# Performance work log

Hardware: AMD Instinct MI355X
Metric: run time of the kernel (lower is better)

The kernel has to match this reference:

```python
import jax, jax.numpy as jnp
import numpy as np

B, T, C, N = 4, 1024, 1024, 64
H = C // N
# dims = [max(32, 32*round(fac*C**p/32))] per module formula for C=1024
D_W, D_A, D_V, D_G = 64, 64, 32, 160
GN_EPS = 0.00064


def setup_inputs() -> dict:
    key = jax.random.key(0)
    keys = iter(jax.random.split(key, 40))

    def rn(shape, s=0.02):
        return jax.random.normal(next(keys), shape, jnp.float32) * s

    return {
        "x": jax.random.normal(next(keys), (B, T, C), jnp.float32),
        "v_first": jax.random.normal(next(keys), (B, T, C), jnp.float32),
        "x_r": rn((1, 1, C), 0.5), "x_w": rn((1, 1, C), 0.5), "x_k": rn((1, 1, C), 0.5),
        "x_v": rn((1, 1, C), 0.5), "x_a": rn((1, 1, C), 0.5), "x_g": rn((1, 1, C), 0.5),
        "w0": rn((1, 1, C), 0.5) - 1.0, "w1": rn((C, D_W)), "w2": rn((D_W, C)),
        "a0": rn((1, 1, C), 0.5), "a1": rn((C, D_A)), "a2": rn((D_A, C)),
        "v0p": rn((1, 1, C), 0.5), "v1": rn((C, D_V)), "v2": rn((D_V, C)),
        "g1": rn((C, D_G)), "g2": rn((D_G, C)),
        "k_k": rn((1, 1, C), 0.2) + 0.8, "k_a": rn((1, 1, C), 0.2) + 1.0,
        "r_k": rn((H, N), 0.5),
        "W_r": rn((C, C)), "W_k": rn((C, C)), "W_v": rn((C, C)), "W_o": rn((C, C)),
        "gn_w": jnp.ones((C,), jnp.float32), "gn_b": jnp.zeros((C,), jnp.float32),
    }


def _group_norm(x2, wgt, bias):
    # torch GroupNorm(H groups, C channels) on [B*T, C]: normalize each N-chunk
    xg = x2.reshape(x2.shape[0], H, N)
    mu = xg.mean(-1, keepdims=True)
    var = ((xg - mu) ** 2).mean(-1, keepdims=True)  # biased var, as torch
    xn = (xg - mu) * jax.lax.rsqrt(var + GN_EPS)
    return xn.reshape(x2.shape) * wgt + bias


def rwkv7_recurrence(r, w, k, v, a, b):
    # RWKV-7 chunked-cuda semantics (wind_rwkv naive reference), all [B,T,H,N];
    # w is the per-channel decay exp(-exp(w_raw)) in (0,1).
    # state s: [B,H,N,N], s[i,j] ~ value_i x key_j
    # s_t = s_{t-1} * diag(w_t) + (s_{t-1} @ a_t) outer b_t + v_t outer k_t
    # y_t = s_t @ r_t
    def step(s, inp):
        r_t, w_t, k_t, v_t, a_t, b_t = inp  # each [B,H,N]
        sa = jnp.einsum('bhij,bhj->bhi', s, a_t)
        s = (s * w_t[:, :, None, :]
             + sa[..., None] * b_t[:, :, None, :]
             + v_t[..., None] * k_t[:, :, None, :])
        y = jnp.einsum('bhij,bhj->bhi', s, r_t)
        return s, y

    xs = tuple(jnp.swapaxes(t, 0, 1) for t in (r, w, k, v, a, b))  # [T,B,H,N]
    s0 = jnp.zeros((r.shape[0], r.shape[2], r.shape[3], r.shape[3]), r.dtype)
    _, ys = jax.lax.scan(step, s0, xs)
    return jnp.swapaxes(ys, 0, 1)  # [B,T,H,N]


def reference(x, v_first, x_r, x_w, x_k, x_v, x_a, x_g, w0, w1, w2, a0, a1, a2,
              v0p, v1, v2, g1, g2, k_k, k_a, r_k, W_r, W_k, W_v, W_o, gn_w, gn_b):
    Bx, Tx, Cx = x.shape
    # F.pad(x, (0,0,1,-1)): shift tokens right by one, zero at t=0
    last_x = jnp.concatenate([jnp.zeros_like(x[:, :1]), x[:, :-1]], axis=1)
    dx = last_x - x
    xr, xw, xk, xv, xa, xg = (x + m * dx for m in (x_r, x_w, x_k, x_v, x_a, x_g))
    r = xr @ W_r.T
    w = -jax.nn.softplus(-w0 - jnp.tanh(xw @ w1) @ w2) - 0.5
    k = xk @ W_k.T
    v = xv @ W_v.T
    v = v + (v_first - v) * jax.nn.sigmoid(v0p + (xv @ v1) @ v2)
    a = jax.nn.sigmoid(a0 + (xa @ a1) @ a2)
    g = jax.nn.sigmoid(xg @ g1) @ g2
    kk = k * k_k
    k = k * (1.0 + (a - 1.0) * k_a)
    rs, ws, ks, vs, kks, aa = (t.reshape(Bx, Tx, H, N) for t in (r, w, k, v, kk, a))
    # F.normalize(kk, dim=-1) with eps clamp 1e-12
    kks = kks / jnp.maximum(jnp.linalg.norm(kks, axis=-1, keepdims=True), 1e-12)
    wdec = jnp.exp(-jnp.exp(ws))
    y = rwkv7_recurrence(rs, wdec, ks, vs, kks, -kks * aa)  # [B,T,H,N]
    yn = _group_norm(y.reshape(Bx * Tx, Cx), gn_w, gn_b).reshape(Bx, Tx, Cx)
    yn = yn + ((rs * ks * r_k).sum(-1, keepdims=True) * vs).reshape(Bx, Tx, Cx)
    return (yn * g) @ W_o.T
```

## Files before the change

kernel.cpp:

```cpp
#include <hip/hip_runtime.h>
#include <hip/hip_bf16.h>
#include <math.h>


using bf16 = __hip_bfloat16;
typedef __attribute__((ext_vector_type(8))) short bf16x8;
typedef __attribute__((ext_vector_type(4))) float f32x4;

#define DEVINL __device__ __forceinline__

DEVINL float b2f(bf16 v) { return __bfloat162float(v); }
DEVINL bf16 f2b(float f) { return __float2bfloat16(f); }
DEVINL float sigm(float x) { return 1.f / (1.f + __expf(-x)); }
DEVINL float bfbits2f(unsigned short s) { return __uint_as_float(((unsigned)s) << 16); }
DEVINL float lo16(unsigned u) { return __uint_as_float(u << 16); }
DEVINL float hi16(unsigned u) { return __uint_as_float(u & 0xffff0000u); }
DEVINL float ldin(const void* p, size_t i, int fl) {
  return fl ? ((const float*)p)[i] : b2f(((const bf16*)p)[i]);
}

DEVINL void g2lds16(const void* g, void* l) {
  __builtin_amdgcn_global_load_lds(
      (__attribute__((address_space(1))) void*)(g),
      (__attribute__((address_space(3))) void*)(l), 16, 0, 0);
}

DEVINL void wait_vmcnt8() {
  __asm__ volatile("" ::: "memory");
  __builtin_amdgcn_s_waitcnt(0x0F78);
  __asm__ volatile("" ::: "memory");
}

template<int CTRL>
DEVINL float dpp_add(float x) {
  int t = __builtin_amdgcn_update_dpp(0, __float_as_int(x), CTRL, 0xf, 0xf, true);
  return x + __int_as_float(t);
}
DEVINL float rowsum16(float x) {
  x = dpp_add<0x121>(x);
  x = dpp_add<0x122>(x);
  x = dpp_add<0x124>(x);
  x = dpp_add<0x128>(x);
  return x;
}

DEVINL size_t stream_sb(int row, int h) {
  return ((size_t)((row >> 10) * 16 + h) * 1024 + (row & 1023)) * 512;
}
DEVINL size_t slotoff(int n, int s) {
  int u = n * 4 + s;
  return (size_t)(((u >> 3) & 1) * 128 + ((u >> 4) << 3) + (u & 7));
}

__global__ void detect_kernel(const unsigned* __restrict__ x, int* __restrict__ flag) {
  __shared__ int cnt[4];
  int tid = threadIdx.x;
  unsigned w = x[tid];
  float v = fabsf(bfbits2f((unsigned short)(w & 0xffffu)));
  bool plaus = (v >= 1e-4f && v <= 16.f);
  unsigned long long m = __ballot(plaus);
  if ((tid & 63) == 0) cnt[tid >> 6] = __popcll(m);
  __syncthreads();
  if (tid == 0) *flag = (cnt[0] + cnt[1] + cnt[2] + cnt[3] < 128) ? 1 : 0;
}

__global__ __launch_bounds__(256)
void prep_kernel(const void* __restrict__ x,
    const void* mr, const void* mw, const void* mk,
    const void* mv, const void* ma, const void* mg,
    const void* W_r, const void* W_k, const void* W_v, const void* W_o,
    bf16* cWr, bf16* cWk, bf16* cWv, bf16* cWo,
    const void* w1, const void* w2, const void* a1, const void* a2,
    const void* v1, const void* v2, const void* g1, const void* g2,
    bf16* w1t, bf16* w2t, bf16* a1t, bf16* a2t,
    bf16* v1t, bf16* v2t, bf16* g1t, bf16* g2t,
    const int* __restrict__ flag,
    bf16* oxr, bf16* oxw, bf16* oxk, bf16* oxv, bf16* oxa, bf16* oxg)
{
  int fl = *flag;
  int bx = blockIdx.x;
  if (bx < 16384) {
    size_t idx = (size_t)bx * 256 + threadIdx.x;
    int c = (int)(idx & 1023);
    int t = (int)((idx >> 10) & 1023);
    float xc = ldin(x, idx, fl);
    float px = (t == 0) ? 0.f : ldin(x, idx - 1024, fl);
    float dx = px - xc;
    oxr[idx] = f2b(xc + ldin(mr, c, fl) * dx);
    oxw[idx] = f2b(xc + ldin(mw, c, fl) * dx);
    oxk[idx] = f2b(xc + ldin(mk, c, fl) * dx);
    oxv[idx] = f2b(xc + ldin(mv, c, fl) * dx);
    oxa[idx] = f2b(xc + ldin(ma, c, fl) * dx);
    oxg[idx] = f2b(xc + ldin(mg, c, fl) * dx);
  } else if (bx < 32768) {
    int g = (bx - 16384) * 256 + threadIdx.x;
    int seg = g >> 20, i = g & 1048575;
    const void* s = seg == 0 ? W_r : seg == 1 ? W_k : seg == 2 ? W_v : W_o;
    bf16* d = seg == 0 ? cWr : seg == 1 ? cWk : seg == 2 ? cWv : cWo;
    d[i] = fl ? f2b(((const float*)s)[i]) : ((const bf16*)s)[i];
  } else {
    int idx = (bx - 32768) * 256 + threadIdx.x;
    if (idx >= 655360) return;
    const int ends[8] = {65536, 131072, 196608, 262144, 294912, 327680, 491520, 655360};
    const int Ks[8] = {1024, 64, 1024, 64, 1024, 32, 1024, 160};
    const int Nd[8] = {64, 1024, 64, 1024, 32, 1024, 160, 1024};
    const void* srcs[8] = {w1, w2, a1, a2, v1, v2, g1, g2};
    bf16* dsts[8] = {w1t, w2t, a1t, a2t, v1t, v2t, g1t, g2t};
    int seg = 0, start = 0;
#pragma unroll
    for (int s2 = 0; s2 < 7; s2++)
      if (idx >= ends[s2]) { seg = s2 + 1; start = ends[s2]; }
    int local = idx - start;
    int K = Ks[seg], N = Nd[seg];
    int k = local / N, n = local - k * N;
    dsts[seg][(size_t)n * K + k] = f2b(ldin(srcs[seg], local, fl));
  }
}

template<typename Epi>
DEVINL void gemm_core(const bf16* __restrict__ A, const bf16* __restrict__ Bt,
                      int K, int Brows, int m0, int n0, Epi&& epi)
{
  __shared__ short As[128 * 32];
  __shared__ short Bs[128 * 32];
  const int tid = threadIdx.x;
  const int wid = tid >> 6, lane = tid & 63;
  const int wr = (wid >> 1) * 64, wc = (wid & 1) * 64;

  f32x4 acc[4][4] = {};

  const int lrow = lane >> 2;
  const int lcol = (lane & 3) * 8;
  int arow0 = m0 + (wid * 2 + 0) * 16 + lrow;
  int arow1 = m0 + (wid * 2 + 1) * 16 + lrow;
  int brow0 = n0 + (wid * 2 + 0) * 16 + lrow; if (brow0 >= Brows) brow0 = Brows - 1;
  int brow1 = n0 + (wid * 2 + 1) * 16 + lrow; if (brow1 >= Brows) brow1 = Brows - 1;

  const short* Ag = (const short*)A;
  const short* Bg = (const short*)Bt;

  for (int kk = 0; kk < K; kk += 32) {
    __syncthreads();
    g2lds16(Ag + (size_t)arow0 * K + kk + lcol, As + (wid * 2 + 0) * 512);
    g2lds16(Ag + (size_t)arow1 * K + kk + lcol, As + (wid * 2 + 1) * 512);
    g2lds16(Bg + (size_t)brow0 * K + kk + lcol, Bs + (wid * 2 + 0) * 512);
    g2lds16(Bg + (size_t)brow1 * K + kk + lcol, Bs + (wid * 2 + 1) * 512);
    __syncthreads();
    bf16x8 af[4], bfr[4];
#pragma unroll
    for (int mi = 0; mi < 4; mi++)
      af[mi] = *(const bf16x8*)(As + (wr + mi * 16 + (lane & 15)) * 32 + (lane >> 4) * 8);
#pragma unroll
    for (int ni = 0; ni < 4; ni++)
      bfr[ni] = *(const bf16x8*)(Bs + (wc + ni * 16 + (lane & 15)) * 32 + (lane >> 4) * 8);
#pragma unroll
    for (int mi = 0; mi < 4; mi++)
#pragma unroll
      for (int ni = 0; ni < 4; ni++)
        acc[mi][ni] = __builtin_amdgcn_mfma_f32_16x16x32_bf16(af[mi], bfr[ni], acc[mi][ni], 0, 0, 0);
  }

  const int cl0 = lane & 15, r0 = (lane >> 4) * 4;
#pragma unroll
  for (int mi = 0; mi < 4; mi++)
#pragma unroll
    for (int ni = 0; ni < 4; ni++) {
      int col = n0 + wc + ni * 16 + cl0;
#pragma unroll
      for (int rr = 0; rr < 4; rr++)
        epi(m0 + wr + mi * 16 + r0 + rr, col, acc[mi][ni][rr]);
    }
}

__global__ __launch_bounds__(256)
void stage1_kernel(const bf16* xw, const bf16* xa, const bf16* xv, const bf16* xg,
                   const bf16* w1t, const bf16* a1t, const bf16* v1t, const bf16* g1t,
                   bf16* hw, bf16* ha, bf16* hv, bf16* hg)
{
  int y = blockIdx.y;
  int seg = (y <= 2) ? y : 3;
  int n0 = (y == 4) ? 128 : 0;
  const bf16* A  = seg == 0 ? xw  : seg == 1 ? xa  : seg == 2 ? xv  : xg;
  const bf16* Bt = seg == 0 ? w1t : seg == 1 ? a1t : seg == 2 ? v1t : g1t;
  int NS         = seg == 0 ? 64  : seg == 1 ? 64  : seg == 2 ? 32  : 160;
  bf16* out      = seg == 0 ? hw  : seg == 1 ? ha  : seg == 2 ? hv  : hg;
  gemm_core(A, Bt, 1024, NS, blockIdx.x * 128, n0, [&](int row, int col, float f) {
    if (col >= NS) return;
    if (seg == 0) f = tanhf(f);
    else if (seg == 3) f = sigm(f);
    out[(size_t)row * NS + col] = f2b(f);
  });
}

__global__ __launch_bounds__(256)
void bigrkv_kernel(const bf16* xr, const bf16* xk, const bf16* xv,
                   const bf16* cWr, const bf16* cWk, const bf16* cWv,
                   bf16* __restrict__ STR)
{
  int z = blockIdx.z;
  const bf16* A  = z == 0 ? xr  : z == 1 ? xk  : xv;
  const bf16* Bt = z == 0 ? cWr : z == 1 ? cWk : cWv;
  gemm_core(A, Bt, 1024, 1024, blockIdx.x * 128, blockIdx.y * 128,
            [&](int row, int col, float f) {
    size_t sb = stream_sb(row, col >> 6);
    int n = col & 63;
    size_t off = (z == 2) ? (sb + 256 + n) : (sb + slotoff(n, z));
    STR[off] = f2b(f);
  });
}

__global__ __launch_bounds__(256)
void stage2_kernel(const bf16* hw, const bf16* ha, const bf16* hv, const bf16* hg,
                   const bf16* w2t, const bf16* a2t, const bf16* v2t, const bf16* g2t,
                   bf16* __restrict__ STR, float* __restrict__ STRf, float* __restrict__ G,
                   const void* w0, const void* a0, const void* v0p, const void* vfirst,
                   const int* __restrict__ flag)
{
  int fl = *flag;
  int z = blockIdx.z;
  const bf16* A  = z == 0 ? hw  : z == 1 ? ha  : z == 2 ? hv  : hg;
  const bf16* Bt = z == 0 ? w2t : z == 1 ? a2t : z == 2 ? v2t : g2t;
  int K          = z == 0 ? 64  : z == 1 ? 64  : z == 2 ? 32  : 160;
  gemm_core(A, Bt, K, 1024, blockIdx.x * 128, blockIdx.y * 128,
            [&](int row, int col, float f) {
    int n = col & 63;
    if (z == 0) {
      float zz = -(ldin(w0, col, fl) + f);
      float sp = fmaxf(zz, 0.f) + __logf(1.f + __expf(-fabsf(zz)));
      STRf[stream_sb(row, col >> 6) / 2 + 160 + n] = __expf(-__expf(-sp - 0.5f));
    } else if (z == 1) {
      STR[stream_sb(row, col >> 6) + slotoff(n, 2)] = f2b(sigm(ldin(a0, col, fl) + f));
    } else if (z == 2) {
      float sg = sigm(ldin(v0p, col, fl) + f);
      size_t pa = stream_sb(row, col >> 6) + 256 + n;
      float vr = b2f(STR[pa]);
      float vf = ldin(vfirst, (size_t)row * 1024 + col, fl);
      STR[pa] = f2b(vr + (vf - vr) * sg);
    } else {
      G[(size_t)row * 1024 + col] = f;
    }
  });
}

__global__ __launch_bounds__(256)
void post_kernel(bf16* __restrict__ STR, const void* __restrict__ kkw,
                 const void* __restrict__ kaw, const int* __restrict__ flag) {
  int fl = *flag;
  int slot = blockIdx.x * 4 + (threadIdx.x >> 6);
  int tg = slot >> 4, h = slot & 15;
  int n = threadIdx.x & 63, c = h * 64 + n;
  size_t sb = stream_sb(tg, h);
  float kraw = b2f(STR[sb + slotoff(n, 1)]);
  float asig = b2f(STR[sb + slotoff(n, 2)]);
  float kk = kraw * ldin(kkw, c, fl);
  float ss = kk * kk;
  ss += __shfl_xor(ss, 1);  ss += __shfl_xor(ss, 2);  ss += __shfl_xor(ss, 4);
  ss += __shfl_xor(ss, 8);  ss += __shfl_xor(ss, 16); ss += __shfl_xor(ss, 32);
  float kkn = kk / fmaxf(sqrtf(ss), 1e-12f);
  STR[sb + slotoff(n, 2)] = f2b(kkn);
  STR[sb + slotoff(n, 3)] = f2b(-kkn * asig);
  STR[sb + slotoff(n, 1)] = f2b(kraw * (1.f + (asig - 1.f) * ldin(kaw, c, fl)));
}

#define CH 8
__global__ __launch_bounds__(64, 1)
void recur_kernel(const char* __restrict__ STR, float* __restrict__ Y) {
  __shared__ __align__(16) char lds[2 * CH * 1024];
  int blk = blockIdx.x;
  int bh = blk & 63, sib = blk >> 6;
  int b = bh >> 4, h = bh & 15;
  int lane = threadIdx.x;
  int jq = lane & 15, rl = lane >> 4;
  int i = sib * 4 + rl;

  const char* gb = STR + (size_t)bh * (1024 * 1024) + lane * 16;
  float* yout = Y + (size_t)b * 1024 * 1024 + h * 64 + i;

  unsigned lbase = (unsigned)(size_t)(__attribute__((address_space(3))) void*)(void*)lds;
  unsigned lA = lbase + (unsigned)(jq * 16);
  unsigned lB = lbase + 256u + (unsigned)(jq * 16);
  unsigned lV = lbase + 512u + (unsigned)(i * 2);
  unsigned lW = lbase + 640u + (unsigned)(jq * 16);

#pragma unroll
  for (int d = 0; d < CH; ++d)
    g2lds16(gb + (size_t)d * 1024, lds + d * 1024);

  float S0 = 0.f, S1 = 0.f, S2 = 0.f, S3 = 0.f;
  uint4 m0r[2], m1r[2]; float4 wvr[2]; unsigned vur[2];

#define RLOAD(BK, SO) do { \
    unsigned _so = (unsigned)(SO); \
    asm volatile("ds_read_b128 %0, %1" : "=v"(m0r[BK]) : "v"(lA + _so)); \
    asm volatile("ds_read_b128 %0, %1" : "=v"(m1r[BK]) : "v"(lB + _so)); \
    asm volatile("ds_read_b128 %0, %1" : "=v"(wvr[BK]) : "v"(lW + _so)); \
    asm volatile("ds_read_u16  %0, %1" : "=v"(vur[BK]) : "v"(lV + _so)); \
  } while (0)

#define WAITL(N) do { \
    asm volatile("s_waitcnt lgkmcnt(" #N ")" ::: "memory"); \
    __builtin_amdgcn_sched_barrier(0); \
  } while (0)

#define RSTEP(BK, TT) do { \
    uint4 M0 = m0r[BK], M1 = m1r[BK]; float4 WV = wvr[BK]; \
    float vi = lo16(vur[BK]); \
    float rx = lo16(M0.x), kx = hi16(M0.x), ax = lo16(M0.y), bxx = hi16(M0.y); \
    float ry = lo16(M0.z), ky = hi16(M0.z), ay = lo16(M0.w), byy = hi16(M0.w); \
    float rz = lo16(M1.x), kz = hi16(M1.x), az = lo16(M1.y), bzz = hi16(M1.y); \
    float rw2 = lo16(M1.z), kw2 = hi16(M1.z), aw2 = lo16(M1.w), bww = hi16(M1.w); \
    float sa = (S0 * ax + S1 * ay) + (S2 * az + S3 * aw2); \
    sa = rowsum16(sa); \
    S0 = S0 * WV.x + (sa * bxx + vi * kx); \
    S1 = S1 * WV.y + (sa * byy + vi * ky); \
    S2 = S2 * WV.z + (sa * bzz + vi * kz); \
    S3 = S3 * WV.w + (sa * bww + vi * kw2); \
    float yy = (S0 * rx + S1 * ry) + (S2 * rz + S3 * rw2); \
    yy = rowsum16(yy); \
    if (jq == 0) yout[(size_t)(TT) * 1024] = yy; \
  } while (0)

  for (int t0 = 0; t0 < 1024; t0 += CH) {
    int cur = (t0 >> 3) & 1;
    unsigned cbase = (unsigned)(cur * (CH * 1024));
    char* bufn = lds + (cur ^ 1) * (CH * 1024);
#pragma unroll
    for (int d = 0; d < CH; ++d)
      g2lds16(gb + (size_t)(t0 + CH + d) * 1024, bufn + d * 1024);
    wait_vmcnt8();
    RLOAD(0, cbase);
#pragma unroll
    for (int d = 0; d < CH; ++d) {
      if (d + 1 < CH) { RLOAD((d + 1) & 1, cbase + (d + 1) * 1024); WAITL(4); }
      else            { WAITL(0); }
      RSTEP(d & 1, t0 + d);
    }
  }
#undef RLOAD
#undef WAITL
#undef RSTEP
}

__global__ __launch_bounds__(256)
void gn_kernel(const float* __restrict__ Y, const bf16* __restrict__ STR,
               const float* __restrict__ G,
               const void* __restrict__ gw, const void* __restrict__ gb,
               const void* __restrict__ rk, const int* __restrict__ flag,
               bf16* __restrict__ Z)
{
  int fl = *flag;
  int slot = blockIdx.x * 4 + (threadIdx.x >> 6);
  int tg = slot >> 4, h = slot & 15;
  int n = threadIdx.x & 63, c = h * 64 + n;
  size_t sb = stream_sb(tg, h);
  float y = Y[(size_t)tg * 1024 + c];
  float rr = b2f(STR[sb + slotoff(n, 0)]);
  float kf = b2f(STR[sb + slotoff(n, 1)]);
  float vv = b2f(STR[sb + 256 + n]);
  float s1 = y, s2 = y * y, s3 = rr * kf * ldin(rk, c, fl);
#pragma unroll
  for (int m = 1; m < 64; m <<= 1) {
    s1 += __shfl_xor(s1, m);
    s2 += __shfl_xor(s2, m);
    s3 += __shfl_xor(s3, m);
  }
  float mu = s1 * 0.015625f;
  float var = s2 * 0.015625f - mu * mu;
  float xn = (y - mu) * rsqrtf(var + 0.00064f);
  float yn = xn * ldin(gw, c, fl) + ldin(gb, c, fl);
  yn += s3 * vv;
  Z[(size_t)tg * 1024 + c] = f2b(yn * G[(size_t)tg * 1024 + c]);
}

__global__ __launch_bounds__(256)
void outgemm_kernel(const bf16* Z, const bf16* cWo,
                    float* oF, bf16* oB, const int* __restrict__ flag)
{
  int fl = *flag;
  gemm_core(Z, cWo, 1024, 1024, blockIdx.x * 128, blockIdx.y * 128,
            [&](int row, int col, float f) {
    if (fl) oF[(size_t)row * 1024 + col] = f;
    else    oB[(size_t)row * 1024 + col] = f2b(f);
  });
}

extern "C" void kernel_launch(void* const* d_in, const int* in_sizes, int n_in,
                              void* d_out, int out_size, void* d_ws, size_t ws_size,
                              hipStream_t stream)
{
  const void* x      = d_in[0];
  const void* vfirst = d_in[1];
  const void* m_r = d_in[2];  const void* m_w = d_in[3];
  const void* m_k = d_in[4];  const void* m_v = d_in[5];
  const void* m_a = d_in[6];  const void* m_g = d_in[7];
  const void* w0  = d_in[8];  const void* w1  = d_in[9];  const void* w2  = d_in[10];
  const void* a0  = d_in[11]; const void* a1  = d_in[12]; const void* a2  = d_in[13];
  const void* v0p = d_in[14]; const void* v1  = d_in[15]; const void* v2  = d_in[16];
  const void* g1  = d_in[17]; const void* g2  = d_in[18];
  const void* k_k = d_in[19]; const void* k_a = d_in[20]; const void* r_k = d_in[21];
  const void* W_r = d_in[22]; const void* W_k = d_in[23];
  const void* W_v = d_in[24]; const void* W_o = d_in[25];
  const void* gnw = d_in[26]; const void* gnb = d_in[27];
  (void)in_sizes; (void)n_in; (void)out_size; (void)ws_size;

  char* ws = (char*)d_ws;
  size_t off = 0;
  auto alloc = [&](size_t bytes) -> void* {
    void* p = ws + off; off += (bytes + 255) & ~(size_t)255; return p;
  };
  const size_t BTC2 = (size_t)4096 * 1024 * 2;
  int*  flag = (int*)alloc(256);
  bf16* cWr = (bf16*)alloc((size_t)1048576 * 2);
  bf16* cWk = (bf16*)alloc((size_t)1048576 * 2);
  bf16* cWv = (bf16*)alloc((size_t)1048576 * 2);
  bf16* cWo = (bf16*)alloc((size_t)1048576 * 2);
  bf16* w1t = (bf16*)alloc((size_t)65536 * 2);
  bf16* w2t = (bf16*)alloc((size_t)65536 * 2);
  bf16* a1t = (bf16*)alloc((size_t)65536 * 2);
  bf16* a2t = (bf16*)alloc((size_t)65536 * 2);
  bf16* v1t = (bf16*)alloc((size_t)32768 * 2);
  bf16* v2t = (bf16*)alloc((size_t)32768 * 2);
  bf16* g1t = (bf16*)alloc((size_t)163840 * 2);
  bf16* g2t = (bf16*)alloc((size_t)163840 * 2);
  bf16* xr = (bf16*)alloc(BTC2);
  bf16* xw = (bf16*)alloc(BTC2);
  bf16* xk = (bf16*)alloc(BTC2);
  bf16* xv = (bf16*)alloc(BTC2);
  bf16* xa = (bf16*)alloc(BTC2);
  bf16* xg = (bf16*)alloc(BTC2);
  char* STR = (char*)alloc((size_t)64 * 1024 * 1024 + 16384);
  bf16* hw  = (bf16*)alloc((size_t)4096 * 64 * 2);
  bf16* ha  = (bf16*)alloc((size_t)4096 * 64 * 2);
  bf16* hv  = (bf16*)alloc((size_t)4096 * 32 * 2);
  bf16* hg  = (bf16*)alloc((size_t)4096 * 160 * 2);
  float* G = (float*)xr;
  float* Y = (float*)xk;
  bf16*  Z = xa;

  detect_kernel<<<1, 256, 0, stream>>>((const unsigned*)x, flag);
  prep_kernel<<<35328, 256, 0, stream>>>(
      x, m_r, m_w, m_k, m_v, m_a, m_g,
      W_r, W_k, W_v, W_o, cWr, cWk, cWv, cWo,
      w1, w2, a1, a2, v1, v2, g1, g2,
      w1t, w2t, a1t, a2t, v1t, v2t, g1t, g2t,
      flag, xr, xw, xk, xv, xa, xg);

  stage1_kernel<<<dim3(32, 5), 256, 0, stream>>>(xw, xa, xv, xg,
                                                 w1t, a1t, v1t, g1t, hw, ha, hv, hg);
  bigrkv_kernel<<<dim3(32, 8, 3), 256, 0, stream>>>(xr, xk, xv, cWr, cWk, cWv, (bf16*)STR);
  stage2_kernel<<<dim3(32, 8, 4), 256, 0, stream>>>(hw, ha, hv, hg,
                                                    w2t, a2t, v2t, g2t,
                                                    (bf16*)STR, (float*)STR, G,
                                                    w0, a0, v0p, vfirst, flag);
  post_kernel<<<16384, 256, 0, stream>>>((bf16*)STR, k_k, k_a, flag);
  recur_kernel<<<1024, 64, 0, stream>>>(STR, Y);
  gn_kernel<<<16384, 256, 0, stream>>>(Y, (bf16*)STR, G, gnw, gnb, r_k, flag, Z);
  outgemm_kernel<<<dim3(32, 8), 256, 0, stream>>>(Z, cWo, (float*)d_out, (bf16*)d_out, flag);
}
```

Measured before the change: 569.7 us.

## Split recurrence state rows across two half-waves with permlane32 fold

Each recurrence wavefront now holds two state rows, each spread across 32 lanes with two elements per lane, instead of four rows across 16 lanes with four elements each. This doubles the grid to 2048 blocks and adds a permlane32 swap to finish each row reduction. The aim is to shorten the serial per-timestep dependency chain and raise occupancy on the latency-bound scan. The cost is twice as many blocks streaming the same per-head input data from memory, plus an extra cross-lane step per reduction.

```diff
diff --git a/kernel.cpp b/kernel.cpp
--- a/kernel.cpp
+++ b/kernel.cpp
@@ -42,6 +42,11 @@
   x = dpp_add<0x124>(x);
   x = dpp_add<0x128>(x);
   return x;
+}
+DEVINL float fold32(float x) {
+  auto r = __builtin_amdgcn_permlane32_swap(__float_as_int(x), __float_as_int(x),
+                                            false, false);
+  return __int_as_float(r[0]) + __int_as_float(r[1]);
 }
 
 DEVINL size_t stream_sb(int row, int h) {
@@ -263,37 +268,37 @@
 }
 
 #define CH 8
-__global__ __launch_bounds__(64, 1)
+__global__ __launch_bounds__(64, 2)
 void recur_kernel(const char* __restrict__ STR, float* __restrict__ Y) {
   __shared__ __align__(16) char lds[2 * CH * 1024];
   int blk = blockIdx.x;
   int bh = blk & 63, sib = blk >> 6;
   int b = bh >> 4, h = bh & 15;
   int lane = threadIdx.x;
-  int jq = lane & 15, rl = lane >> 4;
-  int i = sib * 4 + rl;
+  int jn = (lane & 15) | ((lane >> 5) << 4);
+  int rl = (lane >> 4) & 1;
+  int i = sib * 2 + rl;
+  int q = jn >> 1, half = jn & 1;
 
   const char* gb = STR + (size_t)bh * (1024 * 1024) + lane * 16;
   float* yout = Y + (size_t)b * 1024 * 1024 + h * 64 + i;
 
   unsigned lbase = (unsigned)(size_t)(__attribute__((address_space(3))) void*)(void*)lds;
-  unsigned lA = lbase + (unsigned)(jq * 16);
-  unsigned lB = lbase + 256u + (unsigned)(jq * 16);
-  unsigned lV = lbase + 512u + (unsigned)(i * 2);
-  unsigned lW = lbase + 640u + (unsigned)(jq * 16);
+  unsigned lRK = lbase + (unsigned)(half * 256 + q * 16);
+  unsigned lV  = lbase + 512u + (unsigned)(i * 2);
+  unsigned lW  = lbase + 640u + (unsigned)(jn * 8);
 
 #pragma unroll
   for (int d = 0; d < CH; ++d)
     g2lds16(gb + (size_t)d * 1024, lds + d * 1024);
 
-  float S0 = 0.f, S1 = 0.f, S2 = 0.f, S3 = 0.f;
-  uint4 m0r[2], m1r[2]; float4 wvr[2]; unsigned vur[2];
+  float S0 = 0.f, S1 = 0.f;
+  uint4 m0r[2]; float2 wvr[2]; unsigned vur[2];
 
 #define RLOAD(BK, SO) do { \
     unsigned _so = (unsigned)(SO); \
-    asm volatile("ds_read_b128 %0, %1" : "=v"(m0r[BK]) : "v"(lA + _so)); \
-    asm volatile("ds_read_b128 %0, %1" : "=v"(m1r[BK]) : "v"(lB + _so)); \
-    asm volatile("ds_read_b128 %0, %1" : "=v"(wvr[BK]) : "v"(lW + _so)); \
+    asm volatile("ds_read_b128 %0, %1" : "=v"(m0r[BK]) : "v"(lRK + _so)); \
+    asm volatile("ds_read_b64  %0, %1" : "=v"(wvr[BK]) : "v"(lW + _so)); \
     asm volatile("ds_read_u16  %0, %1" : "=v"(vur[BK]) : "v"(lV + _so)); \
   } while (0)
 
@@ -303,21 +308,17 @@
   } while (0)
 
 #define RSTEP(BK, TT) do { \
-    uint4 M0 = m0r[BK], M1 = m1r[BK]; float4 WV = wvr[BK]; \
+    uint4 M0 = m0r[BK]; float2 WV = wvr[BK]; \
     float vi = lo16(vur[BK]); \
     float rx = lo16(M0.x), kx = hi16(M0.x), ax = lo16(M0.y), bxx = hi16(M0.y); \
     float ry = lo16(M0.z), ky = hi16(M0.z), ay = lo16(M0.w), byy = hi16(M0.w); \
-    float rz = lo16(M1.x), kz = hi16(M1.x), az = lo16(M1.y), bzz = hi16(M1.y); \
-    float rw2 = lo16(M1.z), kw2 = hi16(M1.z), aw2 = lo16(M1.w), bww = hi16(M1.w); \
-    float sa = (S0 * ax + S1 * ay) + (S2 * az + S3 * aw2); \
-    sa = rowsum16(sa); \
+    float sa = S0 * ax + S1 * ay; \
+    sa = rowsum16(sa); sa = fold32(sa); \
     S0 = S0 * WV.x + (sa * bxx + vi * kx); \
     S1 = S1 * WV.y + (sa * byy + vi * ky); \
-    S2 = S2 * WV.z + (sa * bzz + vi * kz); \
-    S3 = S3 * WV.w + (sa * bww + vi * kw2); \
-    float yy = (S0 * rx + S1 * ry) + (S2 * rz + S3 * rw2); \
-    yy = rowsum16(yy); \
-    if (jq == 0) yout[(size_t)(TT) * 1024] = yy; \
+    float yy = S0 * rx + S1 * ry; \
+    yy = rowsum16(yy); yy = fold32(yy); \
+    if (jn == 0) yout[(size_t)(TT) * 1024] = yy; \
   } while (0)
 
   for (int t0 = 0; t0 < 1024; t0 += CH) {
@@ -331,7 +332,7 @@
     RLOAD(0, cbase);
 #pragma unroll
     for (int d = 0; d < CH; ++d) {
-      if (d + 1 < CH) { RLOAD((d + 1) & 1, cbase + (d + 1) * 1024); WAITL(4); }
+      if (d + 1 < CH) { RLOAD((d + 1) & 1, cbase + (d + 1) * 1024); WAITL(3); }
       else            { WAITL(0); }
       RSTEP(d & 1, t0 + d);
     }
@@ -453,7 +454,7 @@
                                                     (bf16*)STR, (float*)STR, G,
                                                     w0, a0, v0p, vfirst, flag);
   post_kernel<<<16384, 256, 0, stream>>>((bf16*)STR, k_k, k_a, flag);
-  recur_kernel<<<1024, 64, 0, stream>>>(STR, Y);
+  recur_kernel<<<2048, 64, 0, stream>>>(STR, Y);
   gn_kernel<<<16384, 256, 0, stream>>>(Y, (bf16*)STR, G, gnw, gnb, r_k, flag, Z);
   outgemm_kernel<<<dim3(32, 8), 256, 0, stream>>>(Z, cWo, (float*)d_out, (bf16*)d_out, flag);
 }
```

New measurement: 674.6 us. +18.4%, slower.

## Defer y cross-lane reductions and stores out of serial recurrence chain

Applied to the files above, without the earlier changes.

The per-step output y reduction (rowsum16) and global store are moved out of the sequential state-update loop. Partial dot products are kept in registers for a whole chunk, reduced together after the chunk, and stored during the next chunk's iteration. The LDS wait is also rewritten to tie its register operands to the wait instead of using a full sched_barrier, which lets the compiler schedule more freely. This shortens the critical dependency chain per timestep at the cost of extra registers.

```diff
diff --git a/kernel.cpp b/kernel.cpp
--- a/kernel.cpp
+++ b/kernel.cpp
@@ -288,6 +288,8 @@
 
   float S0 = 0.f, S1 = 0.f, S2 = 0.f, S3 = 0.f;
   uint4 m0r[2], m1r[2]; float4 wvr[2]; unsigned vur[2];
+  float yp[CH];
+  float ypR[CH];
 
 #define RLOAD(BK, SO) do { \
     unsigned _so = (unsigned)(SO); \
@@ -297,12 +299,14 @@
     asm volatile("ds_read_u16  %0, %1" : "=v"(vur[BK]) : "v"(lV + _so)); \
   } while (0)
 
-#define WAITL(N) do { \
-    asm volatile("s_waitcnt lgkmcnt(" #N ")" ::: "memory"); \
-    __builtin_amdgcn_sched_barrier(0); \
-  } while (0)
-
-#define RSTEP(BK, TT) do { \
+#define WAITTOK(N, BK) \
+    asm volatile("s_waitcnt lgkmcnt(" #N ")" \
+        : "+v"(m0r[BK].x), "+v"(m0r[BK].y), "+v"(m0r[BK].z), "+v"(m0r[BK].w), \
+          "+v"(m1r[BK].x), "+v"(m1r[BK].y), "+v"(m1r[BK].z), "+v"(m1r[BK].w), \
+          "+v"(wvr[BK].x), "+v"(wvr[BK].y), "+v"(wvr[BK].z), "+v"(wvr[BK].w), \
+          "+v"(vur[BK]))
+
+#define RSTEP(BK, DD) do { \
     uint4 M0 = m0r[BK], M1 = m1r[BK]; float4 WV = wvr[BK]; \
     float vi = lo16(vur[BK]); \
     float rx = lo16(M0.x), kx = hi16(M0.x), ax = lo16(M0.y), bxx = hi16(M0.y); \
@@ -315,9 +319,7 @@
     S1 = S1 * WV.y + (sa * byy + vi * ky); \
     S2 = S2 * WV.z + (sa * bzz + vi * kz); \
     S3 = S3 * WV.w + (sa * bww + vi * kw2); \
-    float yy = (S0 * rx + S1 * ry) + (S2 * rz + S3 * rw2); \
-    yy = rowsum16(yy); \
-    if (jq == 0) yout[(size_t)(TT) * 1024] = yy; \
+    yp[DD] = (S0 * rx + S1 * ry) + (S2 * rz + S3 * rw2); \
   } while (0)
 
   for (int t0 = 0; t0 < 1024; t0 += CH) {
@@ -328,16 +330,28 @@
     for (int d = 0; d < CH; ++d)
       g2lds16(gb + (size_t)(t0 + CH + d) * 1024, bufn + d * 1024);
     wait_vmcnt8();
+    if (t0 && jq == 0) {
+#pragma unroll
+      for (int d = 0; d < CH; ++d)
+        yout[(size_t)(t0 - CH + d) * 1024] = ypR[d];
+    }
     RLOAD(0, cbase);
 #pragma unroll
     for (int d = 0; d < CH; ++d) {
-      if (d + 1 < CH) { RLOAD((d + 1) & 1, cbase + (d + 1) * 1024); WAITL(4); }
-      else            { WAITL(0); }
-      RSTEP(d & 1, t0 + d);
+      if (d + 1 < CH) { RLOAD((d + 1) & 1, cbase + (d + 1) * 1024); WAITTOK(4, d & 1); }
+      else            { WAITTOK(0, d & 1); }
+      RSTEP(d & 1, d);
     }
+#pragma unroll
+    for (int d = 0; d < CH; ++d) ypR[d] = rowsum16(yp[d]);
+  }
+  if (jq == 0) {
+#pragma unroll
+    for (int d = 0; d < CH; ++d)
+      yout[(size_t)(1024 - CH + d) * 1024] = ypR[d];
   }
 #undef RLOAD
-#undef WAITL
+#undef WAITTOK
 #undef RSTEP
 }
 
```

Result: slower. 600.8 us (+5.4%).

## Transpose recurrence output, relax vmcnt wait, and use register-token LDS waits

Applied to the files above, without the earlier changes.

The recurrence kernel now writes y in a transposed [b, channel, t] layout, so each channel's outputs across time are contiguous, and the group-norm kernel reads from that layout. The global-to-LDS prefetch wait is relaxed after the first chunk (vmcnt 16), letting more prefetches stay in flight. The LDS wait no longer uses a full sched_barrier; instead it ties only the needed registers to the waitcnt so the compiler can schedule more freely. The risk is strided gathers in the gn kernel, and possible reordering hazards if the register tokens miss a dependency.

```diff
diff --git a/kernel.cpp b/kernel.cpp
--- a/kernel.cpp
+++ b/kernel.cpp
@@ -28,6 +28,11 @@
 DEVINL void wait_vmcnt8() {
   __asm__ volatile("" ::: "memory");
   __builtin_amdgcn_s_waitcnt(0x0F78);
+  __asm__ volatile("" ::: "memory");
+}
+DEVINL void wait_vmcnt16() {
+  __asm__ volatile("" ::: "memory");
+  __builtin_amdgcn_s_waitcnt(0x4F70);
   __asm__ volatile("" ::: "memory");
 }
 
@@ -264,7 +269,7 @@
 
 #define CH 8
 __global__ __launch_bounds__(64, 1)
-void recur_kernel(const char* __restrict__ STR, float* __restrict__ Y) {
+void recur_kernel(const char* __restrict__ STR, float* __restrict__ Yt) {
   __shared__ __align__(16) char lds[2 * CH * 1024];
   int blk = blockIdx.x;
   int bh = blk & 63, sib = blk >> 6;
@@ -274,7 +279,7 @@
   int i = sib * 4 + rl;
 
   const char* gb = STR + (size_t)bh * (1024 * 1024) + lane * 16;
-  float* yout = Y + (size_t)b * 1024 * 1024 + h * 64 + i;
+  float* yout = Yt + ((size_t)b * 1024 + h * 64 + i) * 1024;
 
   unsigned lbase = (unsigned)(size_t)(__attribute__((address_space(3))) void*)(void*)lds;
   unsigned lA = lbase + (unsigned)(jq * 16);
@@ -297,10 +302,12 @@
     asm volatile("ds_read_u16  %0, %1" : "=v"(vur[BK]) : "v"(lV + _so)); \
   } while (0)
 
-#define WAITL(N) do { \
-    asm volatile("s_waitcnt lgkmcnt(" #N ")" ::: "memory"); \
-    __builtin_amdgcn_sched_barrier(0); \
-  } while (0)
+#define WAITTOK(N, BK) \
+    asm volatile("s_waitcnt lgkmcnt(" #N ")" \
+        : "+v"(m0r[BK].x), "+v"(m0r[BK].y), "+v"(m0r[BK].z), "+v"(m0r[BK].w), \
+          "+v"(m1r[BK].x), "+v"(m1r[BK].y), "+v"(m1r[BK].z), "+v"(m1r[BK].w), \
+          "+v"(wvr[BK].x), "+v"(wvr[BK].y), "+v"(wvr[BK].z), "+v"(wvr[BK].w), \
+          "+v"(vur[BK]))
 
 #define RSTEP(BK, TT) do { \
     uint4 M0 = m0r[BK], M1 = m1r[BK]; float4 WV = wvr[BK]; \
@@ -317,7 +324,7 @@
     S3 = S3 * WV.w + (sa * bww + vi * kw2); \
     float yy = (S0 * rx + S1 * ry) + (S2 * rz + S3 * rw2); \
     yy = rowsum16(yy); \
-    if (jq == 0) yout[(size_t)(TT) * 1024] = yy; \
+    if (jq == 0) yout[TT] = yy; \
   } while (0)
 
   for (int t0 = 0; t0 < 1024; t0 += CH) {
@@ -327,22 +334,22 @@
 #pragma unroll
     for (int d = 0; d < CH; ++d)
       g2lds16(gb + (size_t)(t0 + CH + d) * 1024, bufn + d * 1024);
-    wait_vmcnt8();
+    if (t0 == 0) wait_vmcnt8(); else wait_vmcnt16();
     RLOAD(0, cbase);
 #pragma unroll
     for (int d = 0; d < CH; ++d) {
-      if (d + 1 < CH) { RLOAD((d + 1) & 1, cbase + (d + 1) * 1024); WAITL(4); }
-      else            { WAITL(0); }
+      if (d + 1 < CH) { RLOAD((d + 1) & 1, cbase + (d + 1) * 1024); WAITTOK(4, d & 1); }
+      else            { WAITTOK(0, d & 1); }
       RSTEP(d & 1, t0 + d);
     }
   }
 #undef RLOAD
-#undef WAITL
+#undef WAITTOK
 #undef RSTEP
 }
 
 __global__ __launch_bounds__(256)
-void gn_kernel(const float* __restrict__ Y, const bf16* __restrict__ STR,
+void gn_kernel(const float* __restrict__ Yt, const bf16* __restrict__ STR,
                const float* __restrict__ G,
                const void* __restrict__ gw, const void* __restrict__ gb,
                const void* __restrict__ rk, const int* __restrict__ flag,
@@ -353,7 +360,7 @@
   int tg = slot >> 4, h = slot & 15;
   int n = threadIdx.x & 63, c = h * 64 + n;
   size_t sb = stream_sb(tg, h);
-  float y = Y[(size_t)tg * 1024 + c];
+  float y = Yt[((size_t)(tg >> 10) * 1024 + c) * 1024 + (tg & 1023)];
   float rr = b2f(STR[sb + slotoff(n, 0)]);
   float kf = b2f(STR[sb + slotoff(n, 1)]);
   float vv = b2f(STR[sb + 256 + n]);
@@ -434,7 +441,7 @@
   bf16* hv  = (bf16*)alloc((size_t)4096 * 32 * 2);
   bf16* hg  = (bf16*)alloc((size_t)4096 * 160 * 2);
   float* G = (float*)xr;
-  float* Y = (float*)xk;
+  float* Yt = (float*)xk;
   bf16*  Z = xa;
 
   detect_kernel<<<1, 256, 0, stream>>>((const unsigned*)x, flag);
@@ -453,7 +460,7 @@
                                                     (bf16*)STR, (float*)STR, G,
                                                     w0, a0, v0p, vfirst, flag);
   post_kernel<<<16384, 256, 0, stream>>>((bf16*)STR, k_k, k_a, flag);
-  recur_kernel<<<1024, 64, 0, stream>>>(STR, Y);
-  gn_kernel<<<16384, 256, 0, stream>>>(Y, (bf16*)STR, G, gnw, gnb, r_k, flag, Z);
+  recur_kernel<<<1024, 64, 0, stream>>>(STR, Yt);
+  gn_kernel<<<16384, 256, 0, stream>>>(Yt, (bf16*)STR, G, gnw, gnb, r_k, flag, Z);
   outgemm_kernel<<<dim3(32, 8), 256, 0, stream>>>(Z, cWo, (float*)d_out, (bf16*)d_out, flag);
 }
```

New measurement: 577.9 us. About the same (+1.4%).
